# Optimization experiments

Hardware: AMD Instinct MI355X
Metric: run time of the kernel (lower is better)

Reference implementation:

```python
import jax, jax.numpy as jnp
import numpy as np

C_IN, C_HID, N_HEADS = 128, 32, 4
INF = 1.0e9
LN_EPS = 1e-5


def setup_inputs() -> dict:
    key = jax.random.key(0)
    ks = jax.random.split(key, 12)
    B, I, J, C, H, D = 1, 384, 384, C_IN, N_HEADS, C_HID
    s = 0.02
    return {
        "x": jax.random.normal(ks[0], (B, I, J, C), dtype=jnp.float32),
        "mask": jnp.ones((B, I, J), dtype=jnp.float32),
        "ln_g": jnp.ones((C,), dtype=jnp.float32),
        "ln_b": jnp.zeros((C,), dtype=jnp.float32),
        "w_tri": jax.random.normal(ks[1], (C, H), dtype=jnp.float32) * s,
        "wq": jax.random.normal(ks[2], (C, H, D), dtype=jnp.float32) * s,
        "wk": jax.random.normal(ks[3], (C, H, D), dtype=jnp.float32) * s,
        "wv": jax.random.normal(ks[4], (C, H, D), dtype=jnp.float32) * s,
        "wg": jax.random.normal(ks[5], (C, H, D), dtype=jnp.float32) * s,
        "bg": jnp.ones((H, D), dtype=jnp.float32),
        "wo": jax.random.normal(ks[6], (H, D, C), dtype=jnp.float32) * s,
        "bo": jnp.zeros((C,), dtype=jnp.float32),
    }


def reference(x, mask, ln_g, ln_b, w_tri, wq, wk, wv, wg, bg, wo, bo):
    # LayerNorm over channel dim
    mu = jnp.mean(x, axis=-1, keepdims=True)
    var = jnp.mean(jnp.square(x - mu), axis=-1, keepdims=True)
    xn = (x - mu) * jax.lax.rsqrt(var + LN_EPS) * ln_g + ln_b  # [B,I,J,C]

    # mask bias: [B, I, 1, 1, J]
    mask_bias = (INF * (mask - 1.0))[..., :, None, None, :]
    # triangle bias: linear(x) -> [B,I,J,H] -> [B,1,H,I,J]
    tri_bias = jnp.einsum("bijc,ch->bhij", xn, w_tri)[:, None]

    scale = 1.0 / jnp.sqrt(jnp.asarray(C_HID, dtype=xn.dtype))
    # per-row attention over J: tensors [B, I, H, J, D]
    q = jnp.einsum("bixc,chd->bihxd", xn, wq) * scale
    k = jnp.einsum("bixc,chd->bihxd", xn, wk)
    v = jnp.einsum("bixc,chd->bihxd", xn, wv)

    logits = jnp.einsum("bihqd,bihkd->bihqk", q, k) + mask_bias + tri_bias
    a = jax.nn.softmax(logits, axis=-1)
    o = jnp.einsum("bihqk,bihkd->bihqd", a, v)  # [B,I,H,J,D]

    g = jax.nn.sigmoid(jnp.einsum("bixc,chd->bihxd", xn, wg) + bg[None, None, :, None, :])
    o = o * g
    out = jnp.einsum("bihxd,hdc->bixc", o, wo) + bo  # [B,I,J,C]
    return out
```

## Files before the change

### kernel.cpp

```cpp
#include <hip/hip_runtime.h>
#include <math.h>


#define I_DIM 384
#define J_DIM 384
#define C_DIM 128
#define H_DIM 4
#define D_DIM 32
#define NPOS (I_DIM * J_DIM)
#define Q_SCALE 0.17677669529663687f

typedef __attribute__((ext_vector_type(8))) short bf16x8;
typedef __attribute__((ext_vector_type(4))) float f32x4;

__device__ __forceinline__ float sigmoidf_(float v) {
    return 1.0f / (1.0f + __expf(-v));
}
__device__ __forceinline__ unsigned short f2bf(float f) {
    union { float f; unsigned u; } x; x.f = f;
    unsigned u = x.u;
    u += 0x7fffu + ((u >> 16) & 1u);
    return (unsigned short)(u >> 16);
}
__device__ __forceinline__ float bf2f(unsigned short v) {
    union { unsigned u; float f; } x; x.u = ((unsigned)v) << 16;
    return x.f;
}

__global__ __launch_bounds__(256) void prep_kernel(
    const float* __restrict__ wq, const float* __restrict__ wk,
    const float* __restrict__ wv, const float* __restrict__ wg,
    const float* __restrict__ wo, unsigned short* __restrict__ Wt)
{
    const int mat = blockIdx.x;
    const float* W = (mat == 0) ? wq : (mat == 1) ? wk : (mat == 2) ? wv
                    : (mat == 3) ? wg : wo;
    const float scale = (mat == 0) ? Q_SCALE : 1.0f;
    const int t = threadIdx.x;
    const int n = t >> 1, c0 = (t & 1) * 64;
#pragma unroll
    for (int u = 0; u < 8; ++u) {
        unsigned pk[4];
#pragma unroll
        for (int w = 0; w < 4; ++w) {
            const unsigned short a = f2bf(W[(size_t)(c0 + u * 8 + w * 2 + 0) * 128 + n] * scale);
            const unsigned short b = f2bf(W[(size_t)(c0 + u * 8 + w * 2 + 1) * 128 + n] * scale);
            pk[w] = (unsigned)a | ((unsigned)b << 16);
        }
        int4 q; q.x = pk[0]; q.y = pk[1]; q.z = pk[2]; q.w = pk[3];
        *(int4*)(Wt + (size_t)mat * 16384 + n * 128 + c0 + u * 8) = q;
    }
}

__global__ __launch_bounds__(256) void proj_kernel(
    const float* __restrict__ x, const float* __restrict__ ln_g,
    const float* __restrict__ ln_b, const float* __restrict__ w_tri,
    const unsigned short* __restrict__ Wt, const float* __restrict__ bg,
    unsigned short* __restrict__ qb, unsigned short* __restrict__ kb,
    unsigned short* __restrict__ vb, unsigned short* __restrict__ gb,
    float* __restrict__ tri)
{
    __shared__ unsigned short At[128 * 128];
    __shared__ unsigned short Ct[128 * 128];

    const int t = threadIdx.x;
    const int pos0 = blockIdx.x * 128;
    const int lane = t & 63, wave = t >> 6;
    const int q15 = lane & 15, quad = lane >> 4;

    {
        const int g = t >> 2, q = t & 3;
#pragma unroll
        for (int rr = 0; rr < 2; ++rr) {
            const int r = g * 2 + rr;
            const float* xrow = x + (size_t)(pos0 + r) * C_DIM + q * 32;
            float xv[32];
            float s = 0.f, ss = 0.f;
#pragma unroll
            for (int u = 0; u < 8; ++u) {
                float4 v4 = ((const float4*)xrow)[u];
                xv[u * 4 + 0] = v4.x; xv[u * 4 + 1] = v4.y;
                xv[u * 4 + 2] = v4.z; xv[u * 4 + 3] = v4.w;
                s  += v4.x + v4.y + v4.z + v4.w;
                ss += v4.x * v4.x + v4.y * v4.y + v4.z * v4.z + v4.w * v4.w;
            }
            s  += __shfl_xor(s, 1);  s  += __shfl_xor(s, 2);
            ss += __shfl_xor(ss, 1); ss += __shfl_xor(ss, 2);
            const float mu  = s * (1.0f / 128.0f);
            const float var = ss * (1.0f / 128.0f) - mu * mu;
            const float rstd = rsqrtf(var + 1e-5f);

            float ptri[4] = {0.f, 0.f, 0.f, 0.f};
#pragma unroll
            for (int u2 = 0; u2 < 4; ++u2) {
                const int cb = q * 32 + u2 * 8;
                const float4 g0 = *(const float4*)(ln_g + cb);
                const float4 g1 = *(const float4*)(ln_g + cb + 4);
                const float4 b0 = *(const float4*)(ln_b + cb);
                const float4 b1 = *(const float4*)(ln_b + cb + 4);
                float xn8[8];
                xn8[0] = (xv[u2 * 8 + 0] - mu) * rstd * g0.x + b0.x;
                xn8[1] = (xv[u2 * 8 + 1] - mu) * rstd * g0.y + b0.y;
                xn8[2] = (xv[u2 * 8 + 2] - mu) * rstd * g0.z + b0.z;
                xn8[3] = (xv[u2 * 8 + 3] - mu) * rstd * g0.w + b0.w;
                xn8[4] = (xv[u2 * 8 + 4] - mu) * rstd * g1.x + b1.x;
                xn8[5] = (xv[u2 * 8 + 5] - mu) * rstd * g1.y + b1.y;
                xn8[6] = (xv[u2 * 8 + 6] - mu) * rstd * g1.z + b1.z;
                xn8[7] = (xv[u2 * 8 + 7] - mu) * rstd * g1.w + b1.w;
#pragma unroll
                for (int w = 0; w < 8; ++w) {
                    const float4 wt = ((const float4*)w_tri)[cb + w];
                    ptri[0] += xn8[w] * wt.x; ptri[1] += xn8[w] * wt.y;
                    ptri[2] += xn8[w] * wt.z; ptri[3] += xn8[w] * wt.w;
                }
                unsigned pk[4];
#pragma unroll
                for (int w = 0; w < 4; ++w)
                    pk[w] = (unsigned)f2bf(xn8[w * 2]) | ((unsigned)f2bf(xn8[w * 2 + 1]) << 16);
                int4 q4; q4.x = pk[0]; q4.y = pk[1]; q4.z = pk[2]; q4.w = pk[3];
                const int c = q * 4 + u2;
                *(int4*)&At[r * 128 + ((c ^ (r & 7)) * 8)] = q4;
            }
#pragma unroll
            for (int hh = 0; hh < 4; ++hh) {
                ptri[hh] += __shfl_xor(ptri[hh], 1);
                ptri[hh] += __shfl_xor(ptri[hh], 2);
            }
            const int pos = pos0 + r;
            const int i = pos / J_DIM, j = pos - (pos / J_DIM) * J_DIM;
            tri[((size_t)q * I_DIM + i) * J_DIM + j] = ptri[q];
        }
    }
    __syncthreads();

    const int m0 = wave * 32;
    for (int mat = 0; mat < 4; ++mat) {
        const unsigned short* WtM = Wt + (size_t)mat * 16384;

        f32x4 acc[2][8];
#pragma unroll
        for (int mt = 0; mt < 2; ++mt)
#pragma unroll
            for (int nt = 0; nt < 8; ++nt) acc[mt][nt] = (f32x4){0.f, 0.f, 0.f, 0.f};

#pragma unroll
        for (int kk = 0; kk < 4; ++kk) {
            const int sw = ((kk * 4 + quad) ^ (q15 & 7)) * 8;
            const bf16x8 a0 = *(const bf16x8*)&At[(m0 + q15) * 128 + sw];
            const bf16x8 a1 = *(const bf16x8*)&At[(m0 + 16 + q15) * 128 + sw];
            const unsigned short* bp = WtM + q15 * 128 + (kk * 4 + quad) * 8;
#pragma unroll
            for (int nt = 0; nt < 8; ++nt) {
                const bf16x8 b = *(const bf16x8*)(bp + nt * 16 * 128);
                acc[0][nt] = __builtin_amdgcn_mfma_f32_16x16x32_bf16(a0, b, acc[0][nt], 0, 0, 0);
                acc[1][nt] = __builtin_amdgcn_mfma_f32_16x16x32_bf16(a1, b, acc[1][nt], 0, 0, 0);
            }
        }

        __syncthreads();
#pragma unroll
        for (int mt = 0; mt < 2; ++mt)
#pragma unroll
            for (int nt = 0; nt < 8; ++nt) {
                const int col = nt * 16 + q15;
                const float bgl = (mat == 3) ? bg[col] : 0.f;
#pragma unroll
                for (int reg = 0; reg < 4; ++reg) {
                    float v = acc[mt][nt][reg];
                    if (mat == 3) v = sigmoidf_(v + bgl);
                    const int row = m0 + mt * 16 + quad * 4 + reg;
                    Ct[row * 128 + (((col >> 3) ^ (row & 7)) * 8) + (col & 7)] = f2bf(v);
                }
            }
        __syncthreads();
        {
            unsigned short* O = (mat == 0) ? qb : (mat == 1) ? kb : (mat == 2) ? vb : gb;
#pragma unroll
            for (int sgm = 0; sgm < 2; ++sgm) {
                const int ch = t + sgm * 256;
                const int r = ch >> 2, hh = ch & 3;
                const int pos = pos0 + r;
                const int i = pos / J_DIM, j = pos - (pos / J_DIM) * J_DIM;
                unsigned short* dst = O + (((size_t)i * H_DIM + hh) * J_DIM + j) * D_DIM;
#pragma unroll
                for (int w = 0; w < 4; ++w) {
                    const int c = hh * 4 + w;
                    *(int4*)(dst + w * 8) = *(const int4*)&Ct[r * 128 + ((c ^ (r & 7)) * 8)];
                }
            }
        }
    }
}

__global__ __launch_bounds__(256) void tri_tr_kernel(float* __restrict__ tri)
{
    const int h = blockIdx.x / 78;
    int rem = blockIdx.x - h * 78;
    int ti = 0;
    while (rem >= 12 - ti) { rem -= 12 - ti; ++ti; }
    const int tj = ti + rem;

    float* T = tri + (size_t)h * I_DIM * J_DIM;
    __shared__ float A[32][33];
    __shared__ float B[32][33];

    const int t = threadIdx.x;
    const int r = t >> 3, c4 = (t & 7) * 4;

    {
        const float4 v = *(const float4*)(T + (size_t)(ti * 32 + r) * J_DIM + tj * 32 + c4);
        A[r][c4 + 0] = v.x; A[r][c4 + 1] = v.y; A[r][c4 + 2] = v.z; A[r][c4 + 3] = v.w;
        const float4 w = *(const float4*)(T + (size_t)(tj * 32 + r) * J_DIM + ti * 32 + c4);
        B[r][c4 + 0] = w.x; B[r][c4 + 1] = w.y; B[r][c4 + 2] = w.z; B[r][c4 + 3] = w.w;
    }
    __syncthreads();
    {
        float4 v;
        v.x = B[c4 + 0][r]; v.y = B[c4 + 1][r]; v.z = B[c4 + 2][r]; v.w = B[c4 + 3][r];
        *(float4*)(T + (size_t)(ti * 32 + r) * J_DIM + tj * 32 + c4) = v;
        float4 w;
        w.x = A[c4 + 0][r]; w.y = A[c4 + 1][r]; w.z = A[c4 + 2][r]; w.w = A[c4 + 3][r];
        *(float4*)(T + (size_t)(tj * 32 + r) * J_DIM + ti * 32 + c4) = w;
    }
}

__global__ __launch_bounds__(256) void attn_kernel(
    const unsigned short* __restrict__ qb, const unsigned short* __restrict__ kb,
    const unsigned short* __restrict__ vb, unsigned short* gob,
    const float* __restrict__ triT, const float* __restrict__ mask)
{
    __shared__ unsigned short Klds[64 * 32];
    __shared__ unsigned short Vt[32 * 68];
    __shared__ unsigned short Plds[4][32 * 68];
    __shared__ float Mb[J_DIM];

    const int t = threadIdx.x;
    const int lane = t & 63, wave = t >> 6;
    const int q15 = lane & 15, quad = lane >> 4;
    const int i = blockIdx.x >> 2, h = blockIdx.x & 3;
    const size_t hb = (size_t)(i * H_DIM + h) * (J_DIM * D_DIM);
    const int m0 = wave * 96;

    for (int idx = t; idx < J_DIM; idx += 256)
        Mb[idx] = 1.0e9f * (mask[i * J_DIM + idx] - 1.0f);

    bf16x8 qf[6];
#pragma unroll
    for (int m = 0; m < 6; ++m)
        qf[m] = *(const bf16x8*)(qb + hb + (size_t)(m0 + m * 16 + q15) * D_DIM + quad * 8);

    f32x4 Oacc[6][2];
    float sums[6][4];
#pragma unroll
    for (int m = 0; m < 6; ++m) {
#pragma unroll
        for (int d2 = 0; d2 < 2; ++d2) Oacc[m][d2] = (f32x4){0.f, 0.f, 0.f, 0.f};
#pragma unroll
        for (int r = 0; r < 4; ++r) sums[m][r] = 0.f;
    }

    unsigned short* Pw = Plds[wave];
    const float* triH = triT + (size_t)h * J_DIM * I_DIM;

    for (int kt = 0; kt < 6; ++kt) {
        __syncthreads();
        {
            const int kp = t >> 2, du = (t & 3) * 8;
            const size_t gsrc = hb + (size_t)(kt * 64 + kp) * D_DIM + du;
            *(int4*)&Klds[kp * 32 + du] = *(const int4*)(kb + gsrc);
            int4 vv = *(const int4*)(vb + gsrc);
            const unsigned short* vs = (const unsigned short*)&vv;
#pragma unroll
            for (int u = 0; u < 8; ++u)
                Vt[(du + u) * 68 + kp] = vs[u];
        }
        __syncthreads();

        bf16x8 vf[2][2];
#pragma unroll
        for (int ks = 0; ks < 2; ++ks)
#pragma unroll
            for (int d2 = 0; d2 < 2; ++d2)
                vf[ks][d2] = *(const bf16x8*)&Vt[(d2 * 16 + q15) * 68 + ks * 32 + quad * 8];

#pragma unroll
        for (int pass = 0; pass < 3; ++pass) {
            const int mbase = pass * 2;

#pragma unroll
            for (int nt = 0; nt < 4; ++nt) {
                const bf16x8 kf = *(const bf16x8*)&Klds[(nt * 16 + q15) * 32 + quad * 8];
                const float mb = Mb[kt * 64 + nt * 16 + q15];
                const float* tcol = triH + (size_t)(kt * 64 + nt * 16 + q15) * I_DIM;
#pragma unroll
                for (int mm = 0; mm < 2; ++mm) {
                    const int m = mbase + mm;
                    const float4 tb = *(const float4*)(tcol + m0 + m * 16 + quad * 4);
                    f32x4 s = {0.f, 0.f, 0.f, 0.f};
                    s = __builtin_amdgcn_mfma_f32_16x16x32_bf16(qf[m], kf, s, 0, 0, 0);
                    const float p0 = __expf(s[0] + mb + tb.x);
                    const float p1 = __expf(s[1] + mb + tb.y);
                    const float p2 = __expf(s[2] + mb + tb.z);
                    const float p3 = __expf(s[3] + mb + tb.w);
                    sums[m][0] += p0; sums[m][1] += p1;
                    sums[m][2] += p2; sums[m][3] += p3;
                    const int row = mm * 16 + quad * 4;
                    const int col = nt * 16 + q15;
                    Pw[(row + 0) * 68 + col] = f2bf(p0);
                    Pw[(row + 1) * 68 + col] = f2bf(p1);
                    Pw[(row + 2) * 68 + col] = f2bf(p2);
                    Pw[(row + 3) * 68 + col] = f2bf(p3);
                }
            }

#pragma unroll
            for (int mm = 0; mm < 2; ++mm) {
                const int m = mbase + mm;
#pragma unroll
                for (int ks = 0; ks < 2; ++ks) {
                    const bf16x8 af = *(const bf16x8*)&Pw[(mm * 16 + q15) * 68 + ks * 32 + quad * 8];
                    Oacc[m][0] = __builtin_amdgcn_mfma_f32_16x16x32_bf16(af, vf[ks][0], Oacc[m][0], 0, 0, 0);
                    Oacc[m][1] = __builtin_amdgcn_mfma_f32_16x16x32_bf16(af, vf[ks][1], Oacc[m][1], 0, 0, 0);
                }
            }
        }
    }

    float inv[6][4];
#pragma unroll
    for (int m = 0; m < 6; ++m)
#pragma unroll
        for (int r = 0; r < 4; ++r) {
            float s0 = sums[m][r];
            s0 += __shfl_xor(s0, 1); s0 += __shfl_xor(s0, 2);
            s0 += __shfl_xor(s0, 4); s0 += __shfl_xor(s0, 8);
            inv[m][r] = 1.0f / s0;
        }

#pragma unroll
    for (int m = 0; m < 6; ++m) {
        const int qrow = m0 + m * 16 + quad * 4;
#pragma unroll
        for (int d2 = 0; d2 < 2; ++d2) {
            const int d = d2 * 16 + q15;
#pragma unroll
            for (int r = 0; r < 4; ++r) {
                const size_t idx = hb + (size_t)(qrow + r) * D_DIM + d;
                const float g = bf2f(gob[idx]);
                gob[idx] = f2bf(Oacc[m][d2][r] * inv[m][r] * g);
            }
        }
    }
}

__global__ __launch_bounds__(256) void out_kernel(
    const unsigned short* __restrict__ og, const unsigned short* __restrict__ WtO,
    const float* __restrict__ bo, float* __restrict__ out)
{
    __shared__ unsigned short At[128 * 128];
    __shared__ unsigned short Bt[128 * 128];

    const int t = threadIdx.x;
    const int pos0 = blockIdx.x * 128;
    const int lane = t & 63, wave = t >> 6;
    const int q15 = lane & 15, quad = lane >> 4;

    {
        const int r = t >> 1, half = t & 1;
        const int pos = pos0 + r;
        const int i = pos / J_DIM, j = pos - (pos / J_DIM) * J_DIM;
#pragma unroll
        for (int u = 0; u < 8; ++u) {
            const int k0 = half * 64 + u * 8;
            const int hh = k0 >> 5, d0 = k0 & 31;
            const int4 v = *(const int4*)(og + (((size_t)i * H_DIM + hh) * J_DIM + j) * D_DIM + d0);
            const int c = half * 8 + u;
            *(int4*)&At[r * 128 + ((c ^ (r & 7)) * 8)] = v;
        }
        const unsigned short* src = WtO + r * 128 + half * 64;
#pragma unroll
        for (int u = 0; u < 8; ++u) {
            const int c = half * 8 + u;
            *(int4*)&Bt[r * 128 + ((c ^ (r & 7)) * 8)] = *(const int4*)(src + u * 8);
        }
    }
    __syncthreads();

    const int m0 = wave * 32;
    f32x4 acc[2][8];
#pragma unroll
    for (int mt = 0; mt < 2; ++mt)
#pragma unroll
        for (int nt = 0; nt < 8; ++nt) acc[mt][nt] = (f32x4){0.f, 0.f, 0.f, 0.f};

#pragma unroll
    for (int kk = 0; kk < 4; ++kk) {
        const int sw = ((kk * 4 + quad) ^ (q15 & 7)) * 8;
        const bf16x8 a0 = *(const bf16x8*)&At[(m0 + q15) * 128 + sw];
        const bf16x8 a1 = *(const bf16x8*)&At[(m0 + 16 + q15) * 128 + sw];
#pragma unroll
        for (int nt = 0; nt < 8; ++nt) {
            const bf16x8 b = *(const bf16x8*)&Bt[(nt * 16 + q15) * 128 + sw];
            acc[0][nt] = __builtin_amdgcn_mfma_f32_16x16x32_bf16(a0, b, acc[0][nt], 0, 0, 0);
            acc[1][nt] = __builtin_amdgcn_mfma_f32_16x16x32_bf16(a1, b, acc[1][nt], 0, 0, 0);
        }
    }

#pragma unroll
    for (int mt = 0; mt < 2; ++mt)
#pragma unroll
        for (int nt = 0; nt < 8; ++nt) {
            const float bov = bo[nt * 16 + q15];
#pragma unroll
            for (int reg = 0; reg < 4; ++reg) {
                const int pos = pos0 + m0 + mt * 16 + quad * 4 + reg;
                out[(size_t)pos * C_DIM + nt * 16 + q15] = acc[mt][nt][reg] + bov;
            }
        }
}

extern "C" void kernel_launch(void* const* d_in, const int* in_sizes, int n_in,
                              void* d_out, int out_size, void* d_ws, size_t ws_size,
                              hipStream_t stream)
{
    const float* x     = (const float*)d_in[0];
    const float* mask  = (const float*)d_in[1];
    const float* ln_g  = (const float*)d_in[2];
    const float* ln_b  = (const float*)d_in[3];
    const float* w_tri = (const float*)d_in[4];
    const float* wq    = (const float*)d_in[5];
    const float* wk    = (const float*)d_in[6];
    const float* wv    = (const float*)d_in[7];
    const float* wg    = (const float*)d_in[8];
    const float* bg    = (const float*)d_in[9];
    const float* wo    = (const float*)d_in[10];
    const float* bo    = (const float*)d_in[11];
    float* out = (float*)d_out;
    char* ws = (char*)d_ws;

    const size_t NE = (size_t)NPOS * 128;
    unsigned short* qb = (unsigned short*)ws;
    unsigned short* kb = (unsigned short*)(ws + NE * 2);
    unsigned short* vb = (unsigned short*)(ws + NE * 4);
    unsigned short* gb = (unsigned short*)(ws + NE * 6);
    float*         tri = (float*)(ws + NE * 8);
    unsigned short* Wt = (unsigned short*)(ws + NE * 8 + (size_t)NPOS * 4 * 4);

    prep_kernel<<<5, 256, 0, stream>>>(wq, wk, wv, wg, wo, Wt);
    proj_kernel<<<NPOS / 128, 256, 0, stream>>>(x, ln_g, ln_b, w_tri, Wt, bg,
                                                qb, kb, vb, gb, tri);
    tri_tr_kernel<<<H_DIM * 78, 256, 0, stream>>>(tri);
    attn_kernel<<<I_DIM * H_DIM, 256, 0, stream>>>(qb, kb, vb, gb, tri, mask);
    out_kernel<<<NPOS / 128, 256, 0, stream>>>(gb, Wt + 4 * 16384, bo, out);
}
```

Measured before the change: 564.5 us.

## Split LayerNorm from projection GEMM and stage weights in LDS

The fused proj kernel is split in two. A LayerNorm kernel writes normalized bf16 activations plus the triangle bias, and a separate GEMM kernel loads those activations and each weight matrix into swizzled LDS before running MFMA. The aim is to cut register pressure and raise occupancy in each kernel, and to serve B operands from LDS instead of scattered global reads. The cost is an extra bf16 round trip of the activations through global memory and one more kernel launch.

```diff
diff --git a/kernel.cpp b/kernel.cpp
--- a/kernel.cpp
+++ b/kernel.cpp
@@ -52,144 +52,70 @@
     }
 }
 
-__global__ __launch_bounds__(256) void proj_kernel(
+__global__ __launch_bounds__(256) void ln_kernel(
     const float* __restrict__ x, const float* __restrict__ ln_g,
     const float* __restrict__ ln_b, const float* __restrict__ w_tri,
-    const unsigned short* __restrict__ Wt, const float* __restrict__ bg,
-    unsigned short* __restrict__ qb, unsigned short* __restrict__ kb,
-    unsigned short* __restrict__ vb, unsigned short* __restrict__ gb,
-    float* __restrict__ tri)
-{
-    __shared__ unsigned short At[128 * 128];
-    __shared__ unsigned short Ct[128 * 128];
-
-    const int t = threadIdx.x;
-    const int pos0 = blockIdx.x * 128;
-    const int lane = t & 63, wave = t >> 6;
-    const int q15 = lane & 15, quad = lane >> 4;
-
-    {
-        const int g = t >> 2, q = t & 3;
-#pragma unroll
-        for (int rr = 0; rr < 2; ++rr) {
-            const int r = g * 2 + rr;
-            const float* xrow = x + (size_t)(pos0 + r) * C_DIM + q * 32;
-            float xv[32];
-            float s = 0.f, ss = 0.f;
-#pragma unroll
-            for (int u = 0; u < 8; ++u) {
-                float4 v4 = ((const float4*)xrow)[u];
-                xv[u * 4 + 0] = v4.x; xv[u * 4 + 1] = v4.y;
-                xv[u * 4 + 2] = v4.z; xv[u * 4 + 3] = v4.w;
-                s  += v4.x + v4.y + v4.z + v4.w;
-                ss += v4.x * v4.x + v4.y * v4.y + v4.z * v4.z + v4.w * v4.w;
-            }
-            s  += __shfl_xor(s, 1);  s  += __shfl_xor(s, 2);
-            ss += __shfl_xor(ss, 1); ss += __shfl_xor(ss, 2);
-            const float mu  = s * (1.0f / 128.0f);
-            const float var = ss * (1.0f / 128.0f) - mu * mu;
-            const float rstd = rsqrtf(var + 1e-5f);
-
-            float ptri[4] = {0.f, 0.f, 0.f, 0.f};
-#pragma unroll
-            for (int u2 = 0; u2 < 4; ++u2) {
-                const int cb = q * 32 + u2 * 8;
-                const float4 g0 = *(const float4*)(ln_g + cb);
-                const float4 g1 = *(const float4*)(ln_g + cb + 4);
-                const float4 b0 = *(const float4*)(ln_b + cb);
-                const float4 b1 = *(const float4*)(ln_b + cb + 4);
-                float xn8[8];
-                xn8[0] = (xv[u2 * 8 + 0] - mu) * rstd * g0.x + b0.x;
-                xn8[1] = (xv[u2 * 8 + 1] - mu) * rstd * g0.y + b0.y;
-                xn8[2] = (xv[u2 * 8 + 2] - mu) * rstd * g0.z + b0.z;
-                xn8[3] = (xv[u2 * 8 + 3] - mu) * rstd * g0.w + b0.w;
-                xn8[4] = (xv[u2 * 8 + 4] - mu) * rstd * g1.x + b1.x;
-                xn8[5] = (xv[u2 * 8 + 5] - mu) * rstd * g1.y + b1.y;
-                xn8[6] = (xv[u2 * 8 + 6] - mu) * rstd * g1.z + b1.z;
-                xn8[7] = (xv[u2 * 8 + 7] - mu) * rstd * g1.w + b1.w;
-#pragma unroll
-                for (int w = 0; w < 8; ++w) {
-                    const float4 wt = ((const float4*)w_tri)[cb + w];
-                    ptri[0] += xn8[w] * wt.x; ptri[1] += xn8[w] * wt.y;
-                    ptri[2] += xn8[w] * wt.z; ptri[3] += xn8[w] * wt.w;
-                }
-                unsigned pk[4];
-#pragma unroll
-                for (int w = 0; w < 4; ++w)
-                    pk[w] = (unsigned)f2bf(xn8[w * 2]) | ((unsigned)f2bf(xn8[w * 2 + 1]) << 16);
-                int4 q4; q4.x = pk[0]; q4.y = pk[1]; q4.z = pk[2]; q4.w = pk[3];
-                const int c = q * 4 + u2;
-                *(int4*)&At[r * 128 + ((c ^ (r & 7)) * 8)] = q4;
-            }
-#pragma unroll
-            for (int hh = 0; hh < 4; ++hh) {
-                ptri[hh] += __shfl_xor(ptri[hh], 1);
-                ptri[hh] += __shfl_xor(ptri[hh], 2);
-            }
-            const int pos = pos0 + r;
-            const int i = pos / J_DIM, j = pos - (pos / J_DIM) * J_DIM;
-            tri[((size_t)q * I_DIM + i) * J_DIM + j] = ptri[q];
-        }
-    }
-    __syncthreads();
-
-    const int m0 = wave * 32;
-    for (int mat = 0; mat < 4; ++mat) {
-        const unsigned short* WtM = Wt + (size_t)mat * 16384;
-
-        f32x4 acc[2][8];
-#pragma unroll
-        for (int mt = 0; mt < 2; ++mt)
-#pragma unroll
-            for (int nt = 0; nt < 8; ++nt) acc[mt][nt] = (f32x4){0.f, 0.f, 0.f, 0.f};
-
-#pragma unroll
-        for (int kk = 0; kk < 4; ++kk) {
-            const int sw = ((kk * 4 + quad) ^ (q15 & 7)) * 8;
-            const bf16x8 a0 = *(const bf16x8*)&At[(m0 + q15) * 128 + sw];
-            const bf16x8 a1 = *(const bf16x8*)&At[(m0 + 16 + q15) * 128 + sw];
-            const unsigned short* bp = WtM + q15 * 128 + (kk * 4 + quad) * 8;
-#pragma unroll
-            for (int nt = 0; nt < 8; ++nt) {
-                const bf16x8 b = *(const bf16x8*)(bp + nt * 16 * 128);
-                acc[0][nt] = __builtin_amdgcn_mfma_f32_16x16x32_bf16(a0, b, acc[0][nt], 0, 0, 0);
-                acc[1][nt] = __builtin_amdgcn_mfma_f32_16x16x32_bf16(a1, b, acc[1][nt], 0, 0, 0);
-            }
-        }
-
-        __syncthreads();
-#pragma unroll
-        for (int mt = 0; mt < 2; ++mt)
-#pragma unroll
-            for (int nt = 0; nt < 8; ++nt) {
-                const int col = nt * 16 + q15;
-                const float bgl = (mat == 3) ? bg[col] : 0.f;
-#pragma unroll
-                for (int reg = 0; reg < 4; ++reg) {
-                    float v = acc[mt][nt][reg];
-                    if (mat == 3) v = sigmoidf_(v + bgl);
-                    const int row = m0 + mt * 16 + quad * 4 + reg;
-                    Ct[row * 128 + (((col >> 3) ^ (row & 7)) * 8) + (col & 7)] = f2bf(v);
-                }
-            }
-        __syncthreads();
-        {
-            unsigned short* O = (mat == 0) ? qb : (mat == 1) ? kb : (mat == 2) ? vb : gb;
-#pragma unroll
-            for (int sgm = 0; sgm < 2; ++sgm) {
-                const int ch = t + sgm * 256;
-                const int r = ch >> 2, hh = ch & 3;
-                const int pos = pos0 + r;
-                const int i = pos / J_DIM, j = pos - (pos / J_DIM) * J_DIM;
-                unsigned short* dst = O + (((size_t)i * H_DIM + hh) * J_DIM + j) * D_DIM;
-#pragma unroll
-                for (int w = 0; w < 4; ++w) {
-                    const int c = hh * 4 + w;
-                    *(int4*)(dst + w * 8) = *(const int4*)&Ct[r * 128 + ((c ^ (r & 7)) * 8)];
-                }
-            }
-        }
-    }
+    unsigned short* __restrict__ xn, float* __restrict__ tri)
+{
+    const int t = threadIdx.x;
+    const int g = t >> 2, q = t & 3;
+    const int pos = blockIdx.x * 64 + g;
+    const float* xrow = x + (size_t)pos * C_DIM + q * 32;
+
+    float xv[32];
+    float s = 0.f, ss = 0.f;
+#pragma unroll
+    for (int u = 0; u < 8; ++u) {
+        float4 v4 = ((const float4*)xrow)[u];
+        xv[u * 4 + 0] = v4.x; xv[u * 4 + 1] = v4.y;
+        xv[u * 4 + 2] = v4.z; xv[u * 4 + 3] = v4.w;
+        s  += v4.x + v4.y + v4.z + v4.w;
+        ss += v4.x * v4.x + v4.y * v4.y + v4.z * v4.z + v4.w * v4.w;
+    }
+    s  += __shfl_xor(s, 1);  s  += __shfl_xor(s, 2);
+    ss += __shfl_xor(ss, 1); ss += __shfl_xor(ss, 2);
+    const float mu  = s * (1.0f / 128.0f);
+    const float var = ss * (1.0f / 128.0f) - mu * mu;
+    const float rstd = rsqrtf(var + 1e-5f);
+
+    float ptri[4] = {0.f, 0.f, 0.f, 0.f};
+    unsigned short* xdst = xn + (size_t)pos * C_DIM + q * 32;
+#pragma unroll
+    for (int u2 = 0; u2 < 4; ++u2) {
+        const int cb = q * 32 + u2 * 8;
+        const float4 g0 = *(const float4*)(ln_g + cb);
+        const float4 g1 = *(const float4*)(ln_g + cb + 4);
+        const float4 b0 = *(const float4*)(ln_b + cb);
+        const float4 b1 = *(const float4*)(ln_b + cb + 4);
+        float xn8[8];
+        xn8[0] = (xv[u2 * 8 + 0] - mu) * rstd * g0.x + b0.x;
+        xn8[1] = (xv[u2 * 8 + 1] - mu) * rstd * g0.y + b0.y;
+        xn8[2] = (xv[u2 * 8 + 2] - mu) * rstd * g0.z + b0.z;
+        xn8[3] = (xv[u2 * 8 + 3] - mu) * rstd * g0.w + b0.w;
+        xn8[4] = (xv[u2 * 8 + 4] - mu) * rstd * g1.x + b1.x;
+        xn8[5] = (xv[u2 * 8 + 5] - mu) * rstd * g1.y + b1.y;
+        xn8[6] = (xv[u2 * 8 + 6] - mu) * rstd * g1.z + b1.z;
+        xn8[7] = (xv[u2 * 8 + 7] - mu) * rstd * g1.w + b1.w;
+#pragma unroll
+        for (int w = 0; w < 8; ++w) {
+            const float4 wt = ((const float4*)w_tri)[cb + w];
+            ptri[0] += xn8[w] * wt.x; ptri[1] += xn8[w] * wt.y;
+            ptri[2] += xn8[w] * wt.z; ptri[3] += xn8[w] * wt.w;
+        }
+        unsigned pk[4];
+#pragma unroll
+        for (int w = 0; w < 4; ++w)
+            pk[w] = (unsigned)f2bf(xn8[w * 2]) | ((unsigned)f2bf(xn8[w * 2 + 1]) << 16);
+        int4 q4; q4.x = pk[0]; q4.y = pk[1]; q4.z = pk[2]; q4.w = pk[3];
+        *(int4*)(xdst + u2 * 8) = q4;
+    }
+#pragma unroll
+    for (int hh = 0; hh < 4; ++hh) {
+        ptri[hh] += __shfl_xor(ptri[hh], 1);
+        ptri[hh] += __shfl_xor(ptri[hh], 2);
+    }
+    const int i = pos / J_DIM, j = pos - (pos / J_DIM) * J_DIM;
+    tri[((size_t)q * I_DIM + i) * J_DIM + j] = ptri[q];
 }
 
 __global__ __launch_bounds__(256) void tri_tr_kernel(float* __restrict__ tri)
@@ -221,6 +147,98 @@
         float4 w;
         w.x = A[c4 + 0][r]; w.y = A[c4 + 1][r]; w.z = A[c4 + 2][r]; w.w = A[c4 + 3][r];
         *(float4*)(T + (size_t)(tj * 32 + r) * J_DIM + ti * 32 + c4) = w;
+    }
+}
+
+__global__ __launch_bounds__(256) void pgemm_kernel(
+    const unsigned short* __restrict__ xn, const unsigned short* __restrict__ Wt,
+    const float* __restrict__ bg,
+    unsigned short* __restrict__ qb, unsigned short* __restrict__ kb,
+    unsigned short* __restrict__ vb, unsigned short* __restrict__ gb)
+{
+    __shared__ unsigned short At[128 * 128];
+    __shared__ unsigned short Bt[128 * 128];
+
+    const int t = threadIdx.x;
+    const int pos0 = blockIdx.x * 128;
+    const int lane = t & 63, wave = t >> 6;
+    const int q15 = lane & 15, quad = lane >> 4;
+
+    {
+        const int r = t >> 1, half = t & 1;
+        const unsigned short* src = xn + (size_t)(pos0 + r) * C_DIM + half * 64;
+#pragma unroll
+        for (int u = 0; u < 8; ++u) {
+            const int c = half * 8 + u;
+            *(int4*)&At[r * 128 + ((c ^ (r & 7)) * 8)] = *(const int4*)(src + u * 8);
+        }
+    }
+
+    const int m0 = wave * 32;
+    for (int mat = 0; mat < 4; ++mat) {
+        __syncthreads();
+        {
+            const int rn = t >> 1, half = t & 1;
+            const unsigned short* src = Wt + (size_t)mat * 16384 + rn * 128 + half * 64;
+#pragma unroll
+            for (int u = 0; u < 8; ++u) {
+                const int c = half * 8 + u;
+                *(int4*)&Bt[rn * 128 + ((c ^ (rn & 7)) * 8)] = *(const int4*)(src + u * 8);
+            }
+        }
+        __syncthreads();
+
+        f32x4 acc[2][8];
+#pragma unroll
+        for (int mt = 0; mt < 2; ++mt)
+#pragma unroll
+            for (int nt = 0; nt < 8; ++nt) acc[mt][nt] = (f32x4){0.f, 0.f, 0.f, 0.f};
+
+#pragma unroll
+        for (int kk = 0; kk < 4; ++kk) {
+            const int sw = ((kk * 4 + quad) ^ (q15 & 7)) * 8;
+            const bf16x8 a0 = *(const bf16x8*)&At[(m0 + q15) * 128 + sw];
+            const bf16x8 a1 = *(const bf16x8*)&At[(m0 + 16 + q15) * 128 + sw];
+#pragma unroll
+            for (int nt = 0; nt < 8; ++nt) {
+                const bf16x8 b = *(const bf16x8*)&Bt[(nt * 16 + q15) * 128 + sw];
+                acc[0][nt] = __builtin_amdgcn_mfma_f32_16x16x32_bf16(a0, b, acc[0][nt], 0, 0, 0);
+                acc[1][nt] = __builtin_amdgcn_mfma_f32_16x16x32_bf16(a1, b, acc[1][nt], 0, 0, 0);
+            }
+        }
+
+        __syncthreads();
+#pragma unroll
+        for (int mt = 0; mt < 2; ++mt)
+#pragma unroll
+            for (int nt = 0; nt < 8; ++nt) {
+                const int col = nt * 16 + q15;
+                const float bgl = (mat == 3) ? bg[col] : 0.f;
+#pragma unroll
+                for (int reg = 0; reg < 4; ++reg) {
+                    float v = acc[mt][nt][reg];
+                    if (mat == 3) v = sigmoidf_(v + bgl);
+                    const int row = m0 + mt * 16 + quad * 4 + reg;
+                    Bt[row * 128 + (((col >> 3) ^ (row & 7)) * 8) + (col & 7)] = f2bf(v);
+                }
+            }
+        __syncthreads();
+        {
+            unsigned short* O = (mat == 0) ? qb : (mat == 1) ? kb : (mat == 2) ? vb : gb;
+#pragma unroll
+            for (int sgm = 0; sgm < 2; ++sgm) {
+                const int ch = t + sgm * 256;
+                const int r = ch >> 2, hh = ch & 3;
+                const int pos = pos0 + r;
+                const int i = pos / J_DIM, j = pos - (pos / J_DIM) * J_DIM;
+                unsigned short* dst = O + (((size_t)i * H_DIM + hh) * J_DIM + j) * D_DIM;
+#pragma unroll
+                for (int w = 0; w < 4; ++w) {
+                    const int c = hh * 4 + w;
+                    *(int4*)(dst + w * 8) = *(const int4*)&Bt[r * 128 + ((c ^ (r & 7)) * 8)];
+                }
+            }
+        }
     }
 }
 
@@ -445,11 +463,12 @@
     unsigned short* gb = (unsigned short*)(ws + NE * 6);
     float*         tri = (float*)(ws + NE * 8);
     unsigned short* Wt = (unsigned short*)(ws + NE * 8 + (size_t)NPOS * 4 * 4);
+    unsigned short* xn = Wt + 5 * 16384;
 
     prep_kernel<<<5, 256, 0, stream>>>(wq, wk, wv, wg, wo, Wt);
-    proj_kernel<<<NPOS / 128, 256, 0, stream>>>(x, ln_g, ln_b, w_tri, Wt, bg,
-                                                qb, kb, vb, gb, tri);
+    ln_kernel<<<NPOS / 64, 256, 0, stream>>>(x, ln_g, ln_b, w_tri, xn, tri);
     tri_tr_kernel<<<H_DIM * 78, 256, 0, stream>>>(tri);
+    pgemm_kernel<<<NPOS / 128, 256, 0, stream>>>(xn, Wt, bg, qb, kb, vb, gb);
     attn_kernel<<<I_DIM * H_DIM, 256, 0, stream>>>(qb, kb, vb, gb, tri, mask);
     out_kernel<<<NPOS / 128, 256, 0, stream>>>(gb, Wt + 4 * 16384, bo, out);
 }
```

After: 476.7 us. 1.18x faster.
